# Performance work log

Hardware: AMD Instinct MI355X
Metric: run time of the kernel (lower is better)

## Reference

```python
import jax, jax.numpy as jnp
import numpy as np

N, C, T, V = 8, 256, 256, 25
NH = 8
DK = 256           # dk_factor(1.0) * out_channels
DV = 256           # only_temporal_attention -> dv = out_channels
DKH = DK // NH     # 32
DVH = DV // NH     # 32
BN_EPS = 1e-5


def setup_inputs() -> dict:
    key = jax.random.key(0)
    ks = jax.random.split(key, 10)
    return {
        "x": jax.random.normal(ks[0], (N, C, T, V), jnp.float32),
        # pointwise (1,1) qkv conv: weight (2*dk+dv, C), torch conv_init scale
        "qkv_w": jax.random.normal(ks[1], (2 * DK + DV, C), jnp.float32) * (2.0 / (2 * DK + DV)) ** 0.5,
        "qkv_b": jax.random.normal(ks[2], (2 * DK + DV,), jnp.float32) * 0.02,
        # relative key embeddings: (2*frames-1, dk // Nh)
        "key_rel": jax.random.normal(ks[3], (2 * T - 1, DKH), jnp.float32),
        # attn_out pointwise conv: (dv, dv)
        "attn_w": jax.random.normal(ks[4], (DV, DV), jnp.float32) * (1.0 / DV) ** 0.5,
        "attn_b": jax.random.normal(ks[5], (DV,), jnp.float32) * 0.02,
        # BatchNorm2d (eval mode) params / running stats
        "bn_gamma": 1.0 + 0.1 * jax.random.normal(ks[6], (DV,), jnp.float32),
        "bn_beta": 0.1 * jax.random.normal(ks[7], (DV,), jnp.float32),
        "bn_mean": 0.1 * jax.random.normal(ks[8], (DV,), jnp.float32),
        "bn_var": jax.random.uniform(ks[9], (DV,), jnp.float32, minval=0.5, maxval=1.5),
    }


def rel_to_abs(x):
    # x: (B, Nh, L, 2L-1) -> (B, Nh, L, L) via standard pad/reshape/slice trick
    B, Nh, L, _ = x.shape
    x = jnp.pad(x, ((0, 0), (0, 0), (0, 0), (0, 1)))          # (B,Nh,L,2L)
    flat = x.reshape(B, Nh, L * 2 * L)
    flat = jnp.pad(flat, ((0, 0), (0, 0), (0, L - 1)))
    final = flat.reshape(B, Nh, L + 1, 2 * L - 1)
    return final[:, :, :L, L - 1:]


def reference(x, qkv_w, qkv_b, key_rel, attn_w, attn_b, bn_gamma, bn_beta, bn_mean, bn_var):
    n, c, t, v = x.shape
    x_sum = x
    B = n * v
    # (N,C,T,V) -> (N*V, C, T): each joint is an independent temporal sequence
    xr = jnp.transpose(x, (0, 3, 1, 2)).reshape(B, c, t)
    # pointwise qkv conv (kernel (1,1), stride 1)
    qkv = jnp.einsum('bct,oc->bot', xr, qkv_w) + qkv_b[None, :, None]
    q, k, vv = qkv[:, :DK], qkv[:, DK:2 * DK], qkv[:, 2 * DK:]
    q = q.reshape(B, NH, DKH, t) * (DKH ** -0.5)   # scaling applied before rel logits too
    k = k.reshape(B, NH, DKH, t)
    vv = vv.reshape(B, NH, DVH, t)
    # content logits: (B,NH,t,t)
    logits = jnp.einsum('bhdt,bhds->bhts', q, k)
    # relative logits: (B,NH,t,2t-1) -> abs (B,NH,t,t)
    rel = jnp.einsum('bhdt,md->bhtm', q, key_rel)
    logits = logits + rel_to_abs(rel)
    weights = jax.nn.softmax(logits, axis=-1)
    attn = jnp.einsum('bhts,bhds->bhtd', weights, vv)          # (B,NH,t,DVH)
    # combine heads (head-major channel order) -> (B, DV, t)
    attn = jnp.transpose(attn, (0, 1, 3, 2)).reshape(B, DV, t)
    # attn_out pointwise conv
    attn = jnp.einsum('bct,oc->bot', attn, attn_w) + attn_b[None, :, None]
    # (N*V, DV, T) -> (N, DV, T, V)
    attn = attn.reshape(n, v, DV, t).transpose(0, 2, 3, 1)
    # skip connection (in==out, stride==1 -> identity down path)
    result = attn + x_sum
    # BatchNorm2d in eval mode
    inv = bn_gamma / jnp.sqrt(bn_var + BN_EPS)
    result = result * inv[None, :, None, None] + (bn_beta - bn_mean * inv)[None, :, None, None]
    return jax.nn.relu(result)
```

## Files before the change

### kernel.cpp

```cpp
#include <hip/hip_runtime.h>

#define NB 8
#define CC 256
#define TT 256
#define VV 25

typedef unsigned int u32;
typedef unsigned short u16;
typedef __attribute__((ext_vector_type(8))) short s16x8;
typedef __attribute__((ext_vector_type(4))) float f32x4;

__device__ __forceinline__ float bf2f(u16 u) { return __uint_as_float((u32)u << 16); }
__device__ __forceinline__ u16 f2bf(float f) {
    u32 u = __float_as_uint(f);
    u += 0x7fffu + ((u >> 16) & 1u);
    return (u16)(u >> 16);
}

__device__ __forceinline__ void gload_lds16(const void* g, void* l) {
    __builtin_amdgcn_global_load_lds(
        (const __attribute__((address_space(1))) u32*)g,
        (__attribute__((address_space(3))) u32*)l, 16, 0, 0);
}

__global__ __launch_bounds__(256) void k_transpose_x(const float* __restrict__ x,
                                                     u16* __restrict__ xT) {
    __shared__ u16 L[25 * 32 * 34];
    const int tid = threadIdx.x;
    const int c0 = blockIdx.x * 32;
    const int t0 = blockIdx.y * 32;
    const int n  = blockIdx.z;
    for (int i = tid; i < 25600; i += 256) {
        int ci = i / 800;
        int rem = i - ci * 800;
        int t = rem / 25;
        int v = rem - t * 25;
        float f = x[(((size_t)(n * CC + c0 + ci)) * TT + t0) * VV + rem];
        L[(v * 32 + t) * 34 + ci] = f2bf(f);
    }
    __syncthreads();
    for (int i = tid; i < 12800; i += 256) {
        int row = i >> 4, cp = i & 15;
        int v = row >> 5, t = row & 31;
        u32 val = *(const u32*)&L[row * 34 + cp * 2];
        *(u32*)&xT[(((size_t)(n * VV + v)) * TT + t0 + t) * CC + c0 + cp * 2] = val;
    }
}

__global__ __launch_bounds__(256) void k_pack_krel(const float* __restrict__ kr,
                                                   u16* __restrict__ krb) {
    int g = blockIdx.x * 256 + threadIdx.x;
    if (g >= 16384) return;
    krb[g] = (g < 511 * 32) ? f2bf(kr[g]) : (u16)0;
}

__global__ __launch_bounds__(256) void k_pack_w(const float* __restrict__ qkv_w,
                                                const float* __restrict__ attn_w,
                                                const float* __restrict__ qkv_b,
                                                u16* __restrict__ Wqk,
                                                u16* __restrict__ Wv,
                                                u16* __restrict__ Wo,
                                                float* __restrict__ bqk) {
    const float s = 0.17677669529663687f;
    int g = blockIdx.x * 256 + threadIdx.x;
    if (g < 131072) {
        Wqk[g] = f2bf(qkv_w[g] * (g < 65536 ? s : 1.f));
    } else if (g < 196608) {
        Wv[g - 131072] = f2bf(qkv_w[g]);
    } else if (g < 262144) {
        Wo[g - 196608] = f2bf(attn_w[g - 196608]);
    } else if (g < 262656) {
        int i = g - 262144;
        bqk[i] = qkv_b[i] * (i < 256 ? s : 1.f);
    }
}

__device__ __forceinline__ void gemm_mainloop(const u16* __restrict__ Arow,
                                              const u16* __restrict__ Brow,
                                              u16* At, u16* Bt,
                                              int wave, int lane, f32x4 acc[4][4]) {
    const int srow = lane >> 2, scol = (lane & 3) * 8;
    const int quad = lane >> 4, l15 = lane & 15;
    for (int k0 = 0; k0 < 256; k0 += 32) {
#pragma unroll
        for (int it = 0; it < 2; ++it) {
            int ch = it * 4 + wave;
            gload_lds16(Arow + (size_t)(ch * 16 + srow) * 256 + k0 + scol, At + ch * 512 + lane * 8);
            gload_lds16(Brow + (size_t)(ch * 16 + srow) * 256 + k0 + scol, Bt + ch * 512 + lane * 8);
        }
        __syncthreads();
        s16x8 af[4], bfr[4];
#pragma unroll
        for (int i = 0; i < 4; ++i)
            af[i] = *(const s16x8*)&At[((wave & 1) * 64 + i * 16 + l15) * 32 + quad * 8];
#pragma unroll
        for (int j = 0; j < 4; ++j)
            bfr[j] = *(const s16x8*)&Bt[((wave >> 1) * 64 + j * 16 + l15) * 32 + quad * 8];
#pragma unroll
        for (int i = 0; i < 4; ++i)
#pragma unroll
            for (int j = 0; j < 4; ++j)
                acc[i][j] = __builtin_amdgcn_mfma_f32_16x16x32_bf16(af[i], bfr[j], acc[i][j], 0, 0, 0);
        __syncthreads();
    }
}

__global__ __launch_bounds__(256) void k_gemm_qk(const u16* __restrict__ xT,
                                                 const u16* __restrict__ Wqk,
                                                 const float* __restrict__ bqk,
                                                 u16* __restrict__ qT,
                                                 u16* __restrict__ kT) {
    __shared__ __align__(16) u16 At[128 * 32];
    __shared__ __align__(16) u16 Bt[128 * 32];
    const int tid = threadIdx.x, wave = tid >> 6, lane = tid & 63;
    const int quad = lane >> 4, l15 = lane & 15;
    const int n0 = blockIdx.x * 128;
    const int m0 = blockIdx.y * 128;
    const int b  = blockIdx.z;
    const u16* Arow = xT + (size_t)b * 65536 + (size_t)m0 * 256;
    const u16* Brow = Wqk + (size_t)n0 * 256;
    f32x4 acc[4][4];
#pragma unroll
    for (int i = 0; i < 4; ++i)
#pragma unroll
        for (int j = 0; j < 4; ++j) acc[i][j] = (f32x4){0.f, 0.f, 0.f, 0.f};
    gemm_mainloop(Arow, Brow, At, Bt, wave, lane, acc);

    const bool isq = (n0 < 256);
    u16* base = isq ? qT : kT;
    const int on0 = (isq ? n0 : n0 - 256) + (wave >> 1) * 64;
#pragma unroll
    for (int j = 0; j < 4; ++j) {
        int o = on0 + j * 16 + l15;
        float bias = bqk[(isq ? 0 : 256) + o];
        u16* dcol = base + (size_t)(b * 8 + (o >> 5)) * 8192 + (o & 31);
#pragma unroll
        for (int i = 0; i < 4; ++i) {
            int tbase = m0 + (wave & 1) * 64 + i * 16 + quad * 4;
#pragma unroll
            for (int r = 0; r < 4; ++r)
                dcol[(size_t)(tbase + r) * 32] = f2bf(acc[i][j][r] + bias);
        }
    }
}

__global__ __launch_bounds__(256) void k_gemm_av(const u16* __restrict__ Wb,
                                                 const float* __restrict__ bias,
                                                 const u16* __restrict__ Bsrc,
                                                 u16* __restrict__ Out) {
    __shared__ __align__(16) u16 At[128 * 32];
    __shared__ __align__(16) u16 Bt[128 * 32];
    const int tid = threadIdx.x, wave = tid >> 6, lane = tid & 63;
    const int quad = lane >> 4, l15 = lane & 15;
    const int n0 = blockIdx.x * 128;
    const int m0 = blockIdx.y * 128;
    const int b  = blockIdx.z;
    const u16* Arow = Wb + (size_t)m0 * 256;
    const u16* Brow = Bsrc + (size_t)b * 65536 + (size_t)n0 * 256;
    f32x4 acc[4][4];
#pragma unroll
    for (int i = 0; i < 4; ++i)
#pragma unroll
        for (int j = 0; j < 4; ++j) acc[i][j] = (f32x4){0.f, 0.f, 0.f, 0.f};
    gemm_mainloop(Arow, Brow, At, Bt, wave, lane, acc);

    u16* ob = Out + (size_t)b * 65536;
    const int nb = n0 + (wave >> 1) * 64 + l15;
#pragma unroll
    for (int i = 0; i < 4; ++i) {
        int o_i = m0 + (wave & 1) * 64 + i * 16 + quad * 4;
#pragma unroll
        for (int r = 0; r < 4; ++r) {
            float bv = bias[o_i + r];
            u16* orow = ob + (size_t)(o_i + r) * 256 + nb;
#pragma unroll
            for (int j = 0; j < 4; ++j)
                orow[j * 16] = f2bf(acc[i][j][r] + bv);
        }
    }
}

__global__ __launch_bounds__(256) void k_attention_mfma(const u16* __restrict__ qT,
                                                        const u16* __restrict__ kT,
                                                        const u16* __restrict__ vb,
                                                        const u16* __restrict__ krb,
                                                        u16* __restrict__ attn) {
    __shared__ __align__(16) u16 RP[4][16 * 280];

    const int tid = threadIdx.x;
    const int bh = blockIdx.x;
    const int b = bh >> 3, h = bh & 7;
    const int wave = tid >> 6, lane = tid & 63;
    const int quad = lane >> 4, l15 = lane & 15;
    const int t0w = blockIdx.y * 64 + wave * 16;
    const int tl = quad * 4;

    u16* rp = &RP[wave][0];
    const u16* qg  = qT  + (size_t)bh * 8192;
    const u16* kg  = kT  + (size_t)bh * 8192;
    const u16* vg  = vb  + (size_t)bh * 8192;
    const u16* krg = krb + (size_t)(240 - t0w) * 32;

    s16x8 afrag = *(const s16x8*)(qg + (size_t)(t0w + l15) * 32 + quad * 8);

#pragma unroll
    for (int j = 0; j < 17; ++j) {
        s16x8 bfrag = *(const s16x8*)(krg + (size_t)(j * 16 + l15) * 32 + quad * 8);
        f32x4 c = {0.f, 0.f, 0.f, 0.f};
        c = __builtin_amdgcn_mfma_f32_16x16x32_bf16(afrag, bfrag, c, 0, 0, 0);
        int col = j * 16 + l15;
        rp[(tl + 0) * 280 + col] = f2bf(c[0]);
        rp[(tl + 1) * 280 + col] = f2bf(c[1]);
        rp[(tl + 2) * 280 + col] = f2bf(c[2]);
        rp[(tl + 3) * 280 + col] = f2bf(c[3]);
    }

    f32x4 acc[16];
#pragma unroll
    for (int n = 0; n < 16; ++n) {
        s16x8 kf = *(const s16x8*)(kg + (size_t)(n * 16 + l15) * 32 + quad * 8);
        f32x4 z = {0.f, 0.f, 0.f, 0.f};
        acc[n] = __builtin_amdgcn_mfma_f32_16x16x32_bf16(afrag, kf, z, 0, 0, 0);
    }
#pragma unroll
    for (int n = 0; n < 16; ++n) {
#pragma unroll
        for (int r = 0; r < 4; ++r) {
            int tlr = tl + r;
            acc[n][r] += bf2f(rp[tlr * 280 + (n * 16 + l15 - tlr + 15)]);
        }
    }
    float invr[4];
#pragma unroll
    for (int r = 0; r < 4; ++r) {
        float m = acc[0][r];
#pragma unroll
        for (int n = 1; n < 16; ++n) m = fmaxf(m, acc[n][r]);
#pragma unroll
        for (int off = 1; off < 16; off <<= 1) m = fmaxf(m, __shfl_xor(m, off, 64));
        float s = 0.f;
#pragma unroll
        for (int n = 0; n < 16; ++n) {
            float e = __expf(acc[n][r] - m);
            acc[n][r] = e;
            s += e;
        }
#pragma unroll
        for (int off = 1; off < 16; off <<= 1) s += __shfl_xor(s, off, 64);
        invr[r] = 1.f / s;
    }
#pragma unroll
    for (int n = 0; n < 16; ++n) {
#pragma unroll
        for (int r = 0; r < 4; ++r)
            rp[(tl + r) * 280 + n * 16 + l15] = f2bf(acc[n][r] * invr[r]);
    }

#pragma unroll
    for (int j = 0; j < 2; ++j) {
        f32x4 o = {0.f, 0.f, 0.f, 0.f};
#pragma unroll
        for (int ks = 0; ks < 8; ++ks) {
            s16x8 a  = *(const s16x8*)&rp[l15 * 280 + ks * 32 + quad * 8];
            s16x8 bv = *(const s16x8*)(vg + (size_t)(j * 16 + l15) * 256 + ks * 32 + quad * 8);
            o = __builtin_amdgcn_mfma_f32_16x16x32_bf16(a, bv, o, 0, 0, 0);
        }
        u16* ob = attn + ((size_t)b * 256 + t0w + tl) * 256 + h * 32 + j * 16 + l15;
        ob[0]   = f2bf(o[0]);
        ob[256] = f2bf(o[1]);
        ob[512] = f2bf(o[2]);
        ob[768] = f2bf(o[3]);
    }
}

__global__ __launch_bounds__(256) void k_final(const u16* __restrict__ y,
                                               const float* __restrict__ x,
                                               const float* __restrict__ gamma,
                                               const float* __restrict__ beta,
                                               const float* __restrict__ mean,
                                               const float* __restrict__ var,
                                               float* __restrict__ out) {
    __shared__ float tile[1600];
    const int tid = threadIdx.x;
    const int t0 = blockIdx.x * 64;
    const int o  = blockIdx.y;
    const int n  = blockIdx.z;
    float inv = gamma[o] * rsqrtf(var[o] + 1e-5f);
    float sh  = beta[o] - mean[o] * inv;
    for (int p = tid; p < 1600; p += 256) {
        int v = p >> 6, j = p & 63;
        tile[j * VV + v] = bf2f(y[(((size_t)(n * VV + v)) * CC + o) * TT + t0 + j]);
    }
    __syncthreads();
    size_t gbase = (((size_t)(n * CC + o)) * TT + t0) * VV;
    for (int i = tid; i < 1600; i += 256) {
        float val = tile[i] + x[gbase + i];
        val = val * inv + sh;
        out[gbase + i] = fmaxf(val, 0.f);
    }
}

extern "C" void kernel_launch(void* const* d_in, const int* in_sizes, int n_in,
                              void* d_out, int out_size, void* d_ws, size_t ws_size,
                              hipStream_t stream) {
    const float* x        = (const float*)d_in[0];
    const float* qkv_w    = (const float*)d_in[1];
    const float* qkv_b    = (const float*)d_in[2];
    const float* key_rel  = (const float*)d_in[3];
    const float* attn_w   = (const float*)d_in[4];
    const float* attn_b   = (const float*)d_in[5];
    const float* bn_gamma = (const float*)d_in[6];
    const float* bn_beta  = (const float*)d_in[7];
    const float* bn_mean  = (const float*)d_in[8];
    const float* bn_var   = (const float*)d_in[9];
    float* out = (float*)d_out;

    char* ws = (char*)d_ws;
    u16* xT    = (u16*)ws;
    u16* qT    = (u16*)(ws + 26214400);
    u16* kT    = (u16*)(ws + 52428800);
    u16* vb    = (u16*)(ws + 78643200);
    u16* attnT = (u16*)(ws + 104857600);
    u16* y     = qT;

    char* outc = (char*)d_out;
    u16* Wqk   = (u16*)outc;
    u16* Wv    = (u16*)(outc + 262144);
    u16* Wo    = (u16*)(outc + 393216);
    float* bqk = (float*)(outc + 524288);
    u16* krb   = (u16*)(outc + 526336);

    k_pack_w<<<1026, 256, 0, stream>>>(qkv_w, attn_w, qkv_b, Wqk, Wv, Wo, bqk);
    k_pack_krel<<<64, 256, 0, stream>>>(key_rel, krb);
    k_transpose_x<<<dim3(8, 8, 8), 256, 0, stream>>>(x, xT);
    k_gemm_qk<<<dim3(4, 2, 200), 256, 0, stream>>>(xT, Wqk, bqk, qT, kT);
    k_gemm_av<<<dim3(2, 2, 200), 256, 0, stream>>>(Wv, qkv_b + 512, xT, vb);
    k_attention_mfma<<<dim3(1600, 4), 256, 0, stream>>>(qT, kT, vb, krb, attnT);
    k_gemm_av<<<dim3(2, 2, 200), 256, 0, stream>>>(Wo, attn_b, attnT, y);
    k_final<<<dim3(4, 256, 8), 256, 0, stream>>>(y, x, bn_gamma, bn_beta, bn_mean, bn_var, out);
}
```

Baseline: 345.6 us.

## Store QK row-major interleaved, fuse pack kernels, tree softmax reductions, RTZ bf16

Q and K are now written by the QK GEMM as one row-major [t][512] buffer per sequence, so the epilogue stores coalesced rows instead of scattered per-head columns. The attention kernel reads Q and K from that strided layout. The weight and key_rel packing kernels are merged into one launch. In attention, the relative logits seed the MFMA accumulator directly, the max and sum reductions use tree form, bf16 conversion of intermediates uses truncation instead of round-to-nearest, and launch bounds ask for 4 blocks per CU. The risks are less accurate truncated bf16 values and less contiguous K/Q fragment loads in attention.

```diff
diff --git a/kernel.cpp b/kernel.cpp
--- a/kernel.cpp
+++ b/kernel.cpp
@@ -16,6 +16,7 @@
     u += 0x7fffu + ((u >> 16) & 1u);
     return (u16)(u >> 16);
 }
+__device__ __forceinline__ u16 f2bf_rtz(float f) { return (u16)(__float_as_uint(f) >> 16); }
 
 __device__ __forceinline__ void gload_lds16(const void* g, void* l) {
     __builtin_amdgcn_global_load_lds(
@@ -47,20 +48,15 @@
     }
 }
 
-__global__ __launch_bounds__(256) void k_pack_krel(const float* __restrict__ kr,
-                                                   u16* __restrict__ krb) {
-    int g = blockIdx.x * 256 + threadIdx.x;
-    if (g >= 16384) return;
-    krb[g] = (g < 511 * 32) ? f2bf(kr[g]) : (u16)0;
-}
-
-__global__ __launch_bounds__(256) void k_pack_w(const float* __restrict__ qkv_w,
-                                                const float* __restrict__ attn_w,
-                                                const float* __restrict__ qkv_b,
-                                                u16* __restrict__ Wqk,
-                                                u16* __restrict__ Wv,
-                                                u16* __restrict__ Wo,
-                                                float* __restrict__ bqk) {
+__global__ __launch_bounds__(256) void k_pack_all(const float* __restrict__ qkv_w,
+                                                  const float* __restrict__ attn_w,
+                                                  const float* __restrict__ qkv_b,
+                                                  const float* __restrict__ key_rel,
+                                                  u16* __restrict__ Wqk,
+                                                  u16* __restrict__ Wv,
+                                                  u16* __restrict__ Wo,
+                                                  float* __restrict__ bqk,
+                                                  u16* __restrict__ krb) {
     const float s = 0.17677669529663687f;
     int g = blockIdx.x * 256 + threadIdx.x;
     if (g < 131072) {
@@ -72,6 +68,9 @@
     } else if (g < 262656) {
         int i = g - 262144;
         bqk[i] = qkv_b[i] * (i < 256 ? s : 1.f);
+    } else if (g < 279040) {
+        int i = g - 262656;
+        krb[i] = (i < 511 * 32) ? f2bf(key_rel[i]) : (u16)0;
     }
 }
 
@@ -108,8 +107,7 @@
 __global__ __launch_bounds__(256) void k_gemm_qk(const u16* __restrict__ xT,
                                                  const u16* __restrict__ Wqk,
                                                  const float* __restrict__ bqk,
-                                                 u16* __restrict__ qT,
-                                                 u16* __restrict__ kT) {
+                                                 u16* __restrict__ qk_all) {
     __shared__ __align__(16) u16 At[128 * 32];
     __shared__ __align__(16) u16 Bt[128 * 32];
     const int tid = threadIdx.x, wave = tid >> 6, lane = tid & 63;
@@ -126,20 +124,20 @@
         for (int j = 0; j < 4; ++j) acc[i][j] = (f32x4){0.f, 0.f, 0.f, 0.f};
     gemm_mainloop(Arow, Brow, At, Bt, wave, lane, acc);
 
-    const bool isq = (n0 < 256);
-    u16* base = isq ? qT : kT;
-    const int on0 = (isq ? n0 : n0 - 256) + (wave >> 1) * 64;
-#pragma unroll
-    for (int j = 0; j < 4; ++j) {
-        int o = on0 + j * 16 + l15;
-        float bias = bqk[(isq ? 0 : 256) + o];
-        u16* dcol = base + (size_t)(b * 8 + (o >> 5)) * 8192 + (o & 31);
-#pragma unroll
-        for (int i = 0; i < 4; ++i) {
-            int tbase = m0 + (wave & 1) * 64 + i * 16 + quad * 4;
-#pragma unroll
-            for (int r = 0; r < 4; ++r)
-                dcol[(size_t)(tbase + r) * 32] = f2bf(acc[i][j][r] + bias);
+    u16* ob = qk_all + (size_t)b * 131072;
+    const int nb = n0 + (wave >> 1) * 64 + l15;
+    float bj[4];
+#pragma unroll
+    for (int j = 0; j < 4; ++j) bj[j] = bqk[nb + j * 16];
+#pragma unroll
+    for (int i = 0; i < 4; ++i) {
+        int t_i = m0 + (wave & 1) * 64 + i * 16 + quad * 4;
+#pragma unroll
+        for (int r = 0; r < 4; ++r) {
+            u16* orow = ob + (size_t)(t_i + r) * 512 + nb;
+#pragma unroll
+            for (int j = 0; j < 4; ++j)
+                orow[j * 16] = f2bf(acc[i][j][r] + bj[j]);
         }
     }
 }
@@ -180,11 +178,10 @@
     }
 }
 
-__global__ __launch_bounds__(256) void k_attention_mfma(const u16* __restrict__ qT,
-                                                        const u16* __restrict__ kT,
-                                                        const u16* __restrict__ vb,
-                                                        const u16* __restrict__ krb,
-                                                        u16* __restrict__ attn) {
+__global__ __launch_bounds__(256, 4) void k_attention_mfma(const u16* __restrict__ qk,
+                                                           const u16* __restrict__ vb,
+                                                           const u16* __restrict__ krb,
+                                                           u16* __restrict__ attn) {
     __shared__ __align__(16) u16 RP[4][16 * 280];
 
     const int tid = threadIdx.x;
@@ -196,12 +193,11 @@
     const int tl = quad * 4;
 
     u16* rp = &RP[wave][0];
-    const u16* qg  = qT  + (size_t)bh * 8192;
-    const u16* kg  = kT  + (size_t)bh * 8192;
-    const u16* vg  = vb  + (size_t)bh * 8192;
-    const u16* krg = krb + (size_t)(240 - t0w) * 32;
-
-    s16x8 afrag = *(const s16x8*)(qg + (size_t)(t0w + l15) * 32 + quad * 8);
+    const u16* qrow = qk + (size_t)b * 131072;
+    const u16* vg   = vb + (size_t)bh * 8192;
+    const u16* krg  = krb + (size_t)(240 - t0w) * 32;
+
+    s16x8 afrag = *(const s16x8*)(qrow + (size_t)(t0w + l15) * 512 + h * 32 + quad * 8);
 
 #pragma unroll
     for (int j = 0; j < 17; ++j) {
@@ -209,42 +205,54 @@
         f32x4 c = {0.f, 0.f, 0.f, 0.f};
         c = __builtin_amdgcn_mfma_f32_16x16x32_bf16(afrag, bfrag, c, 0, 0, 0);
         int col = j * 16 + l15;
-        rp[(tl + 0) * 280 + col] = f2bf(c[0]);
-        rp[(tl + 1) * 280 + col] = f2bf(c[1]);
-        rp[(tl + 2) * 280 + col] = f2bf(c[2]);
-        rp[(tl + 3) * 280 + col] = f2bf(c[3]);
+        rp[(tl + 0) * 280 + col] = f2bf_rtz(c[0]);
+        rp[(tl + 1) * 280 + col] = f2bf_rtz(c[1]);
+        rp[(tl + 2) * 280 + col] = f2bf_rtz(c[2]);
+        rp[(tl + 3) * 280 + col] = f2bf_rtz(c[3]);
     }
 
     f32x4 acc[16];
-#pragma unroll
-    for (int n = 0; n < 16; ++n) {
-        s16x8 kf = *(const s16x8*)(kg + (size_t)(n * 16 + l15) * 32 + quad * 8);
-        f32x4 z = {0.f, 0.f, 0.f, 0.f};
-        acc[n] = __builtin_amdgcn_mfma_f32_16x16x32_bf16(afrag, kf, z, 0, 0, 0);
-    }
 #pragma unroll
     for (int n = 0; n < 16; ++n) {
 #pragma unroll
         for (int r = 0; r < 4; ++r) {
             int tlr = tl + r;
-            acc[n][r] += bf2f(rp[tlr * 280 + (n * 16 + l15 - tlr + 15)]);
-        }
-    }
+            acc[n][r] = bf2f(rp[tlr * 280 + (n * 16 + l15 - tlr + 15)]);
+        }
+    }
+#pragma unroll
+    for (int n = 0; n < 16; ++n) {
+        s16x8 kf = *(const s16x8*)(qrow + (size_t)(n * 16 + l15) * 512 + 256 + h * 32 + quad * 8);
+        acc[n] = __builtin_amdgcn_mfma_f32_16x16x32_bf16(afrag, kf, acc[n], 0, 0, 0);
+    }
+
     float invr[4];
 #pragma unroll
     for (int r = 0; r < 4; ++r) {
-        float m = acc[0][r];
-#pragma unroll
-        for (int n = 1; n < 16; ++n) m = fmaxf(m, acc[n][r]);
+        float tmp[16];
+#pragma unroll
+        for (int n = 0; n < 16; ++n) tmp[n] = acc[n][r];
+#pragma unroll
+        for (int st = 8; st; st >>= 1)
+#pragma unroll
+            for (int n = 0; n < 8; ++n)
+                if (n < st) tmp[n] = fmaxf(tmp[n], tmp[n + st]);
+        float m = tmp[0];
 #pragma unroll
         for (int off = 1; off < 16; off <<= 1) m = fmaxf(m, __shfl_xor(m, off, 64));
-        float s = 0.f;
+        float sm[16];
 #pragma unroll
         for (int n = 0; n < 16; ++n) {
             float e = __expf(acc[n][r] - m);
             acc[n][r] = e;
-            s += e;
-        }
+            sm[n] = e;
+        }
+#pragma unroll
+        for (int st = 8; st; st >>= 1)
+#pragma unroll
+            for (int n = 0; n < 8; ++n)
+                if (n < st) sm[n] += sm[n + st];
+        float s = sm[0];
 #pragma unroll
         for (int off = 1; off < 16; off <<= 1) s += __shfl_xor(s, off, 64);
         invr[r] = 1.f / s;
@@ -253,7 +261,7 @@
     for (int n = 0; n < 16; ++n) {
 #pragma unroll
         for (int r = 0; r < 4; ++r)
-            rp[(tl + r) * 280 + n * 16 + l15] = f2bf(acc[n][r] * invr[r]);
+            rp[(tl + r) * 280 + n * 16 + l15] = f2bf_rtz(acc[n][r] * invr[r]);
     }
 
 #pragma unroll
@@ -316,12 +324,11 @@
     float* out = (float*)d_out;
 
     char* ws = (char*)d_ws;
-    u16* xT    = (u16*)ws;
-    u16* qT    = (u16*)(ws + 26214400);
-    u16* kT    = (u16*)(ws + 52428800);
-    u16* vb    = (u16*)(ws + 78643200);
-    u16* attnT = (u16*)(ws + 104857600);
-    u16* y     = qT;
+    u16* xT     = (u16*)ws;
+    u16* qk_all = (u16*)(ws + 26214400);
+    u16* vb     = (u16*)(ws + 78643200);
+    u16* attnT  = (u16*)(ws + 104857600);
+    u16* y      = qk_all;
 
     char* outc = (char*)d_out;
     u16* Wqk   = (u16*)outc;
@@ -330,12 +337,11 @@
     float* bqk = (float*)(outc + 524288);
     u16* krb   = (u16*)(outc + 526336);
 
-    k_pack_w<<<1026, 256, 0, stream>>>(qkv_w, attn_w, qkv_b, Wqk, Wv, Wo, bqk);
-    k_pack_krel<<<64, 256, 0, stream>>>(key_rel, krb);
+    k_pack_all<<<1090, 256, 0, stream>>>(qkv_w, attn_w, qkv_b, key_rel, Wqk, Wv, Wo, bqk, krb);
     k_transpose_x<<<dim3(8, 8, 8), 256, 0, stream>>>(x, xT);
-    k_gemm_qk<<<dim3(4, 2, 200), 256, 0, stream>>>(xT, Wqk, bqk, qT, kT);
+    k_gemm_qk<<<dim3(4, 2, 200), 256, 0, stream>>>(xT, Wqk, bqk, qk_all);
     k_gemm_av<<<dim3(2, 2, 200), 256, 0, stream>>>(Wv, qkv_b + 512, xT, vb);
-    k_attention_mfma<<<dim3(1600, 4), 256, 0, stream>>>(qT, kT, vb, krb, attnT);
+    k_attention_mfma<<<dim3(1600, 4), 256, 0, stream>>>(qk_all, vb, krb, attnT);
     k_gemm_av<<<dim3(2, 2, 200), 256, 0, stream>>>(Wo, attn_b, attnT, y);
     k_final<<<dim3(4, 256, 8), 256, 0, stream>>>(y, x, bn_gamma, bn_beta, bn_mean, bn_var, out);
 }
```

New measurement: 361.2 us. 1.05x slower.
